# Kernel tuning notes

Measured on AMD Instinct MI355X. Metric: run time of the kernel, lower is better.

The kernel has to match this reference:

```python
import jax, jax.numpy as jnp
import numpy as np

EPS = 1e-5

def _rms(x, w):
    # RMSNorm over last dim (head_dim), affine weight w
    v = jnp.mean(jnp.square(x), axis=-1, keepdims=True)
    return x * jax.lax.rsqrt(v + EPS) * w

def _rope(x, cos, sin):
    # x: [B, N, H, D]; cos/sin: [N, D] (interleaved-pair convention)
    xr = x.reshape(*x.shape[:-1], -1, 2)
    rot = jnp.stack([-xr[..., 1], xr[..., 0]], axis=-1).reshape(x.shape)
    return x * cos[None, :, None, :] + rot * sin[None, :, None, :]

def _rope_tables(n, d):
    pos = np.arange(n, dtype=np.float32)
    freqs = 1.0 / (10000.0 ** (np.arange(0, d, 2, dtype=np.float32) / d))
    ang = pos[:, None] * freqs[None, :]          # [n, d/2]
    ang = np.repeat(ang, 2, axis=1)              # [n, d] interleaved pairs
    return jnp.asarray(np.cos(ang)), jnp.asarray(np.sin(ang))

def setup_inputs() -> dict:
    key = jax.random.key(0)
    ks = jax.random.split(key, 6)
    B, N1, N2, C, H, D = 2, 1536, 512, 1024, 16, 64
    cos1, sin1 = _rope_tables(N1, D)
    cos2, sin2 = _rope_tables(N2, D)
    s = 0.02
    return dict(
        seq_len=N1,
        x=jax.random.normal(ks[0], (B, N1, C), jnp.float32),
        y=jax.random.normal(ks[1], (B, N2, C), jnp.float32),
        cos1=cos1, sin1=sin1, cos2=cos2, sin2=sin2,
        W_qkv_xs=jax.random.normal(ks[2], (3 * C, C), jnp.float32) * s,
        W_qkv_au=jax.random.normal(ks[3], (3 * C, C), jnp.float32) * s,
        xs_q_w=jnp.ones((D,), jnp.float32), xs_k_w=jnp.ones((D,), jnp.float32),
        au_q_w=jnp.ones((D,), jnp.float32), au_k_w=jnp.ones((D,), jnp.float32),
        W_xs_proj=jax.random.normal(ks[4], (C, C), jnp.float32) * s,
        b_xs_proj=jnp.zeros((C,), jnp.float32),
        W_au_proj=jax.random.normal(ks[5], (C, C), jnp.float32) * s,
        b_au_proj=jnp.zeros((C,), jnp.float32),
    )

def reference(seq_len, x, y, cos1, sin1, cos2, sin2,
              W_qkv_xs, W_qkv_au, xs_q_w, xs_k_w, au_q_w, au_k_w,
              W_xs_proj, b_xs_proj, W_au_proj, b_au_proj):
    B, N1, C = x.shape
    N2 = y.shape[1]
    D = xs_q_w.shape[0]
    H = C // D
    scale = D ** -0.5

    # visual stream: QKV -> per-head RMSNorm -> RoPE
    xq, xk, xv = jnp.split(x @ W_qkv_xs.T, 3, axis=-1)          # each [B,N1,C]
    xq = _rms(xq.reshape(B, N1, H, D), xs_q_w)
    xk = _rms(xk.reshape(B, N1, H, D), xs_k_w)
    xv = xv.reshape(B, N1, H, D).transpose(0, 2, 1, 3)           # [B,H,N1,D]
    xq = _rope(xq, cos1, sin1).transpose(0, 2, 1, 3)             # [B,H,N1,D]
    xk = _rope(xk, cos1, sin1).transpose(0, 2, 1, 3)

    # audio stream: QKV -> per-head RMSNorm -> RoPE
    aq, ak, av = jnp.split(y @ W_qkv_au.T, 3, axis=-1)
    aq = _rms(aq.reshape(B, N2, H, D), au_q_w)
    ak = _rms(ak.reshape(B, N2, H, D), au_k_w)
    av = av.reshape(B, N2, H, D).transpose(0, 2, 1, 3)           # [B,H,N2,D]
    aq = _rope(aq, cos2, sin2).transpose(0, 2, 1, 3)             # [B,H,N2,D]
    ak = _rope(ak, cos2, sin2).transpose(0, 2, 1, 3)

    # joint attention over concatenated sequence
    q = jnp.concatenate([xq, aq], axis=2)                        # [B,H,N1+N2,D]
    k = jnp.concatenate([xk, ak], axis=2)
    v = jnp.concatenate([xv, av], axis=2)
    attn = jax.nn.softmax(jnp.einsum('bhqd,bhkd->bhqk', q * scale, k), axis=-1)
    o = jnp.einsum('bhqk,bhkd->bhqd', attn, v)
    o = o.transpose(0, 2, 1, 3).reshape(B, N1 + N2, C)

    xs = o[:, :N1] @ W_xs_proj.T + b_xs_proj
    au = o[:, N1:] @ W_au_proj.T + b_au_proj
    return xs, au
```

## Files before the change

kernel.cpp:

```cpp
#include <hip/hip_runtime.h>
#include <hip/hip_bf16.h>

typedef __bf16 bf16_t;
typedef bf16_t bf16x4_t __attribute__((ext_vector_type(4)));
typedef bf16_t bf16x8_t __attribute__((ext_vector_type(8)));
typedef float f32x4_t __attribute__((ext_vector_type(4)));
typedef float f32x16_t __attribute__((ext_vector_type(16)));

constexpr int kB = 2, kN1 = 1536, kN2 = 512, kN = 2048, kC = 1024, kH = 16, kD = 64;
constexpr int BK = 64, LDT = 72;

__device__ inline uint32_t pack2bf(float a, float b) {
  union { bf16_t h[2]; uint32_t u; } t;
  t.h[0] = (bf16_t)a; t.h[1] = (bf16_t)b;
  return t.u;
}
__device__ inline void pl32_swap(uint32_t& a, uint32_t& b) {
  asm volatile("v_permlane32_swap_b32 %0, %1" : "+v"(a), "+v"(b));
}
__device__ __forceinline__ void gl16(const bf16_t* g, bf16_t* l) {
  __builtin_amdgcn_global_load_lds(
      (const __attribute__((address_space(1))) unsigned int*)g,
      (__attribute__((address_space(3))) unsigned int*)l, 16, 0, 0);
}

__global__ __launch_bounds__(256)
void cvt_bf16(const float* __restrict__ x, const float* __restrict__ y,
              const float* __restrict__ wqx, const float* __restrict__ wqa,
              const float* __restrict__ wpx, const float* __restrict__ wpa,
              bf16_t* __restrict__ Xb, bf16_t* __restrict__ Wq, bf16_t* __restrict__ Wp)
{
  const int bid = blockIdx.x;
  const float* src; bf16_t* dst; size_t off;
  if (bid < 192)      { src = x;   dst = Xb;           off = (size_t)bid * 16384; }
  else if (bid < 256) { src = y;   dst = Xb + 3145728; off = (size_t)(bid - 192) * 16384; }
  else if (bid < 448) { src = wqx; dst = Wq;           off = (size_t)(bid - 256) * 16384; }
  else if (bid < 640) { src = wqa; dst = Wq + 3145728; off = (size_t)(bid - 448) * 16384; }
  else if (bid < 704) { src = wpx; dst = Wp;           off = (size_t)(bid - 640) * 16384; }
  else                { src = wpa; dst = Wp + 1048576; off = (size_t)(bid - 704) * 16384; }
  src += off; dst += off;
  const int t = threadIdx.x;
  #pragma unroll
  for (int i = 0; i < 16; ++i) {
    const int e = (t + i * 256) * 4;
    f32x4_t v = *(const f32x4_t*)(src + e);
    bf16x4_t o;
    #pragma unroll
    for (int j = 0; j < 4; ++j) o[j] = (bf16_t)v[j];
    *(bf16x4_t*)(dst + e) = o;
  }
}

__global__ __launch_bounds__(256, 2)
void qkv_gemm(const bf16_t* __restrict__ Xb, const bf16_t* __restrict__ Wq,
              const float* __restrict__ cos1, const float* __restrict__ sin1,
              const float* __restrict__ cos2, const float* __restrict__ sin2,
              const float* __restrict__ xs_qw, const float* __restrict__ xs_kw,
              const float* __restrict__ au_qw, const float* __restrict__ au_kw,
              bf16_t* __restrict__ Qb, bf16_t* __restrict__ Kb, bf16_t* __restrict__ Vt)
{
  __shared__ __align__(16) bf16_t smem[32768];
  const int tid = threadIdx.x, lane = tid & 63, w = tid >> 6;
  const int wr = w >> 1, wc = w & 1;
  const int bm = blockIdx.x, bn = blockIdx.y;
  const int l15 = lane & 15, l4 = (lane >> 4) & 3;
  const int K = kC;
  const bool is_xs = bm < 24;

  const bf16_t* Ag = Xb + (size_t)bm * 128 * K;
  const bf16_t* Bg = Wq + (is_xs ? (size_t)0 : (size_t)3072 * 1024) + (size_t)bn * 128 * K;

  const int srow_l = lane >> 3;
  const int scc = (((lane & 7) ^ ((lane >> 3) & 7)) << 3);

  auto stage = [&](int c, int kt) {
    const int k0 = kt * BK;
    bf16_t* Ab = smem + c * 8192;
    bf16_t* Bb = smem + 16384 + c * 8192;
    #pragma unroll
    for (int i = 0; i < 4; ++i) {
      const int row = w * 32 + i * 8 + srow_l;
      gl16(Ag + (size_t)row * K + k0 + scc, Ab + (w * 32 + i * 8) * 64);
      gl16(Bg + (size_t)row * K + k0 + scc, Bb + (w * 32 + i * 8) * 64);
    }
  };

  f32x4_t acc[4][4] = {};
  const int nk = K / BK;
  stage(0, 0);
  asm volatile("s_waitcnt vmcnt(0)" ::: "memory");
  __syncthreads();

  int cur = 0;
  for (int kt = 0; kt < nk; ++kt) {
    if (kt + 1 < nk) stage(cur ^ 1, kt + 1);
    const bf16_t* Ab = smem + cur * 8192;
    const bf16_t* Bb = smem + 16384 + cur * 8192;
    #pragma unroll
    for (int kk = 0; kk < 2; ++kk) {
      bf16x8_t a[4], b[4];
      #pragma unroll
      for (int m = 0; m < 4; ++m) {
        const int row = wr * 64 + m * 16 + l15;
        const int cc = (kk * 32 + l4 * 8) ^ ((row & 7) << 3);
        a[m] = *(const bf16x8_t*)&Ab[row * 64 + cc];
      }
      #pragma unroll
      for (int n = 0; n < 4; ++n) {
        const int row = wc * 64 + n * 16 + l15;
        const int cc = (kk * 32 + l4 * 8) ^ ((row & 7) << 3);
        b[n] = *(const bf16x8_t*)&Bb[row * 64 + cc];
      }
      #pragma unroll
      for (int m = 0; m < 4; ++m)
        #pragma unroll
        for (int n = 0; n < 4; ++n)
          acc[m][n] = __builtin_amdgcn_mfma_f32_16x16x32_bf16(a[m], b[n], acc[m][n], 0, 0, 0);
    }
    asm volatile("s_waitcnt vmcnt(0)" ::: "memory");
    __syncthreads();
    cur ^= 1;
  }

  const int sec = bn >> 3;
  const int grow0 = bm * 128;
  int b, n0, seq_off; const float* cT; const float* sT;
  if (is_xs) { b = grow0 / 1536; n0 = grow0 - b * 1536; seq_off = 0; cT = cos1; sT = sin1; }
  else { const int g2 = grow0 - 3072; b = g2 >> 9; n0 = g2 & 511; seq_off = 1536; cT = cos2; sT = sin2; }
  const int h = (bn & 7) * 2 + wc;

  if (sec < 2) {
    const float* wsel = is_xs ? (sec == 0 ? xs_qw : xs_kw) : (sec == 0 ? au_qw : au_kw);
    float wv[4];
    #pragma unroll
    for (int n = 0; n < 4; ++n) wv[n] = wsel[n * 16 + l15];
    bf16_t* Out = (sec == 0 ? Qb : Kb) + (((size_t)b * kH + h) * kN + seq_off + n0) * kD;
    const float qscale = (sec == 0) ? 0.125f * 1.44269504088896f : 1.0f;
    #pragma unroll
    for (int m = 0; m < 4; ++m)
      #pragma unroll
      for (int r = 0; r < 4; ++r) {
        const int rl = wr * 64 + m * 16 + l4 * 4 + r;
        float ss = 0.0f;
        #pragma unroll
        for (int n = 0; n < 4; ++n) ss += acc[m][n][r] * acc[m][n][r];
        ss += __shfl_xor(ss, 1); ss += __shfl_xor(ss, 2);
        ss += __shfl_xor(ss, 4); ss += __shfl_xor(ss, 8);
        const float rinv = rsqrtf(ss * (1.0f / 64.0f) + 1e-5f);
        const int nrow = n0 + rl;
        #pragma unroll
        for (int n = 0; n < 4; ++n) {
          const int dd = n * 16 + l15;
          const float xn = acc[m][n][r] * rinv * wv[n];
          const float partner = __shfl_xor(xn, 1);
          if (!(l15 & 1)) {
            const float c = cT[(size_t)nrow * 64 + dd];
            const float s = sT[(size_t)nrow * 64 + dd];
            const float ve = (xn * c - partner * s) * qscale;
            const float vo = (partner * c + xn * s) * qscale;
            *(uint32_t*)&Out[(size_t)rl * kD + dd] = pack2bf(ve, vo);
          }
        }
      }
  } else {
    bf16_t* Lt = smem;
    #pragma unroll
    for (int m = 0; m < 4; ++m)
      #pragma unroll
      for (int n = 0; n < 4; ++n) {
        const int col = wc * 64 + n * 16 + l15;
        #pragma unroll
        for (int j = 0; j < 2; ++j) {
          const int row = wr * 64 + m * 16 + l4 * 4 + j * 2;
          *(uint32_t*)&Lt[col * 136 + row] = pack2bf(acc[m][n][j * 2], acc[m][n][j * 2 + 1]);
        }
      }
    __syncthreads();
    const int seg = tid >> 1, half = tid & 1;
    const int hl = seg >> 6, dd = seg & 63;
    bf16_t* Vo = Vt + (((size_t)b * kH + (bn & 7) * 2 + hl) * kD + dd) * kN
                 + seq_off + n0 + half * 64;
    #pragma unroll
    for (int jj = 0; jj < 8; ++jj)
      *(bf16x8_t*)&Vo[jj * 8] = *(const bf16x8_t*)&Lt[seg * 136 + half * 64 + jj * 8];
  }
}

__global__ __launch_bounds__(256, 2)
void proj_gemm(const bf16_t* __restrict__ Ob, const bf16_t* __restrict__ Wp,
               const float* __restrict__ bxs, const float* __restrict__ bau,
               float* __restrict__ out)
{
  __shared__ __align__(16) bf16_t smem[32768];
  const int tid = threadIdx.x, lane = tid & 63, w = tid >> 6;
  const int wr = w >> 1, wc = w & 1;
  const int bm = blockIdx.x, bn = blockIdx.y;
  const int l15 = lane & 15, l4 = (lane >> 4) & 3;
  const int K = kC, N = kC;

  const int grow = bm * 128;
  const int b = grow >> 11, n0r = grow & 2047;
  const bf16_t* Bg; const float* bias; float* Cg;
  if (n0r < kN1) { Bg = Wp; bias = bxs; Cg = out + ((size_t)b * kN1 + n0r) * kC; }
  else { Bg = Wp + (size_t)1024 * 1024; bias = bau;
         Cg = out + (size_t)kB * kN1 * kC + ((size_t)b * kN2 + (n0r - kN1)) * kC; }
  Bg += (size_t)bn * 128 * K;
  const bf16_t* Ag = Ob + (size_t)grow * K;

  const int srow_l = lane >> 3;
  const int scc = (((lane & 7) ^ ((lane >> 3) & 7)) << 3);

  auto stage = [&](int c, int kt) {
    const int k0 = kt * BK;
    bf16_t* Ab = smem + c * 8192;
    bf16_t* Bb = smem + 16384 + c * 8192;
    #pragma unroll
    for (int i = 0; i < 4; ++i) {
      const int row = w * 32 + i * 8 + srow_l;
      gl16(Ag + (size_t)row * K + k0 + scc, Ab + (w * 32 + i * 8) * 64);
      gl16(Bg + (size_t)row * K + k0 + scc, Bb + (w * 32 + i * 8) * 64);
    }
  };

  f32x4_t acc[4][4] = {};
  const int nk = K / BK;
  stage(0, 0);
  asm volatile("s_waitcnt vmcnt(0)" ::: "memory");
  __syncthreads();

  int cur = 0;
  for (int kt = 0; kt < nk; ++kt) {
    if (kt + 1 < nk) stage(cur ^ 1, kt + 1);
    const bf16_t* Ab = smem + cur * 8192;
    const bf16_t* Bb = smem + 16384 + cur * 8192;
    #pragma unroll
    for (int kk = 0; kk < 2; ++kk) {
      bf16x8_t a[4], bfr[4];
      #pragma unroll
      for (int m = 0; m < 4; ++m) {
        const int row = wr * 64 + m * 16 + l15;
        const int cc = (kk * 32 + l4 * 8) ^ ((row & 7) << 3);
        a[m] = *(const bf16x8_t*)&Ab[row * 64 + cc];
      }
      #pragma unroll
      for (int n = 0; n < 4; ++n) {
        const int row = wc * 64 + n * 16 + l15;
        const int cc = (kk * 32 + l4 * 8) ^ ((row & 7) << 3);
        bfr[n] = *(const bf16x8_t*)&Bb[row * 64 + cc];
      }
      #pragma unroll
      for (int m = 0; m < 4; ++m)
        #pragma unroll
        for (int n = 0; n < 4; ++n)
          acc[m][n] = __builtin_amdgcn_mfma_f32_16x16x32_bf16(a[m], bfr[n], acc[m][n], 0, 0, 0);
    }
    asm volatile("s_waitcnt vmcnt(0)" ::: "memory");
    __syncthreads();
    cur ^= 1;
  }

  float bv[4];
  #pragma unroll
  for (int n = 0; n < 4; ++n) bv[n] = bias[bn * 128 + wc * 64 + n * 16 + l15];
  #pragma unroll
  for (int m = 0; m < 4; ++m)
    #pragma unroll
    for (int n = 0; n < 4; ++n) {
      const int col = bn * 128 + wc * 64 + n * 16 + l15;
      #pragma unroll
      for (int r = 0; r < 4; ++r) {
        const int row = wr * 64 + m * 16 + l4 * 4 + r;
        Cg[(size_t)row * N + col] = acc[m][n][r] + bv[n];
      }
    }
}

__global__ __launch_bounds__(512, 2)
void flash_attn(const bf16_t* __restrict__ Q, const bf16_t* __restrict__ K,
                const bf16_t* __restrict__ Vt, bf16_t* __restrict__ O)
{
  __shared__ __align__(16) bf16_t smem[18432];
  const int tid = threadIdx.x, lane = tid & 63, w = tid >> 6;
  const int l31 = lane & 31, hi8 = ((lane >> 5) << 3), hi4 = ((lane >> 5) << 2);
  const int lin = blockIdx.x;
  const int qt = lin >> 5, hid = lin & 31;
  const int h = hid & 15, b = hid >> 4;
  const size_t headoff = ((size_t)(b * kH + h)) * kN * kD;
  const bf16_t* Kg = K + headoff;
  const bf16_t* Vg = Vt + headoff;

  bf16x8_t qf[4];
  {
    const bf16_t* Qg = Q + headoff + (size_t)(qt * 256 + w * 32 + l31) * kD + hi8;
    #pragma unroll
    for (int ks = 0; ks < 4; ++ks) qf[ks] = *(const bf16x8_t*)(Qg + ks * 16);
  }
  bf16x8_t onesv;
  #pragma unroll
  for (int j = 0; j < 8; ++j) onesv[j] = (bf16_t)1.0f;

  const int srow = tid >> 3, sc = (tid & 7) * 8;
  bf16x8_t kreg = *(const bf16x8_t*)(Kg + srow * kD + sc);
  bf16x8_t vreg = *(const bf16x8_t*)(Vg + (size_t)srow * kN + sc);

  f32x16_t oA0 = {}, oA1 = {}, accl = {};

  for (int kt = 0; kt < kN / 64; ++kt) {
    const int cur = kt & 1;
    bf16_t* Kc = smem + cur * 4608;
    bf16_t* Vc = smem + 9216 + cur * 4608;
    *(bf16x8_t*)&Kc[srow * LDT + sc] = kreg;
    *(bf16x8_t*)&Vc[srow * LDT + sc] = vreg;
    if (kt + 1 < kN / 64) {
      kreg = *(const bf16x8_t*)(Kg + (size_t)(kt + 1) * 64 * kD + srow * kD + sc);
      vreg = *(const bf16x8_t*)(Vg + (size_t)srow * kN + (kt + 1) * 64 + sc);
    }
    __syncthreads();

    f32x16_t s0 = {}, s1 = {};
    #pragma unroll
    for (int ks = 0; ks < 4; ++ks) {
      bf16x8_t k0 = *(const bf16x8_t*)&Kc[l31 * LDT + ks * 16 + hi8];
      bf16x8_t k1 = *(const bf16x8_t*)&Kc[(32 + l31) * LDT + ks * 16 + hi8];
      s0 = __builtin_amdgcn_mfma_f32_32x32x16_bf16(k0, qf[ks], s0, 0, 0, 0);
      s1 = __builtin_amdgcn_mfma_f32_32x32x16_bf16(k1, qf[ks], s1, 0, 0, 0);
    }

    #pragma unroll
    for (int i = 0; i < 16; ++i) {
      s0[i] = __builtin_amdgcn_exp2f(s0[i]);
      s1[i] = __builtin_amdgcn_exp2f(s1[i]);
    }

    union PW { uint32_t wd[4]; bf16x8_t v; } pf[4];
    #pragma unroll
    for (int o = 0; o < 2; ++o) {
      #pragma unroll
      for (int hh = 0; hh < 2; ++hh) {
        const int h8 = hh * 8, ks = o * 2 + hh;
        float p0, p1, p2, p3, p4, p5, p6, p7;
        if (o == 0) {
          p0 = s0[h8+0]; p1 = s0[h8+1]; p2 = s0[h8+2]; p3 = s0[h8+3];
          p4 = s0[h8+4]; p5 = s0[h8+5]; p6 = s0[h8+6]; p7 = s0[h8+7];
        } else {
          p0 = s1[h8+0]; p1 = s1[h8+1]; p2 = s1[h8+2]; p3 = s1[h8+3];
          p4 = s1[h8+4]; p5 = s1[h8+5]; p6 = s1[h8+6]; p7 = s1[h8+7];
        }
        uint32_t xw  = pack2bf(p0, p1), x2 = pack2bf(p2, p3);
        uint32_t yw  = pack2bf(p4, p5), y2 = pack2bf(p6, p7);
        pl32_swap(xw, yw);
        pl32_swap(x2, y2);
        pf[ks].wd[0] = xw; pf[ks].wd[1] = x2; pf[ks].wd[2] = yw; pf[ks].wd[3] = y2;
      }
    }

    #pragma unroll
    for (int ks = 0; ks < 4; ++ks) {
      bf16x8_t v0 = *(const bf16x8_t*)&Vc[l31 * LDT + ks * 16 + hi8];
      bf16x8_t v1 = *(const bf16x8_t*)&Vc[(32 + l31) * LDT + ks * 16 + hi8];
      oA0 = __builtin_amdgcn_mfma_f32_32x32x16_bf16(v0, pf[ks].v, oA0, 0, 0, 0);
      oA1 = __builtin_amdgcn_mfma_f32_32x32x16_bf16(v1, pf[ks].v, oA1, 0, 0, 0);
      accl = __builtin_amdgcn_mfma_f32_32x32x16_bf16(onesv, pf[ks].v, accl, 0, 0, 0);
    }
  }

  __syncthreads();
  bf16_t* Ow = smem + w * 2304;
  const float inv = 1.0f / accl[0];
  #pragma unroll
  for (int db = 0; db < 2; ++db) {
    f32x16_t o = db ? oA1 : oA0;
    #pragma unroll
    for (int rp = 0; rp < 8; ++rp) {
      const int d = db * 32 + ((rp & 1) << 1) + ((rp >> 1) << 3) + hi4;
      *(uint32_t*)&Ow[l31 * LDT + d] = pack2bf(o[2 * rp] * inv, o[2 * rp + 1] * inv);
    }
  }
  const int rq = lane >> 1, half = lane & 1;
  bf16x8_t r0 = *(const bf16x8_t*)&Ow[rq * LDT + half * 32];
  bf16x8_t r1 = *(const bf16x8_t*)&Ow[rq * LDT + half * 32 + 8];
  bf16x8_t r2 = *(const bf16x8_t*)&Ow[rq * LDT + half * 32 + 16];
  bf16x8_t r3 = *(const bf16x8_t*)&Ow[rq * LDT + half * 32 + 24];
  bf16_t* Og = O + ((size_t)b * kN + qt * 256 + w * 32 + rq) * kC + h * kD + half * 32;
  *(bf16x8_t*)&Og[0]  = r0;
  *(bf16x8_t*)&Og[8]  = r1;
  *(bf16x8_t*)&Og[16] = r2;
  *(bf16x8_t*)&Og[24] = r3;
}

extern "C" void kernel_launch(void* const* d_in, const int* in_sizes, int n_in,
                              void* d_out, int out_size, void* d_ws, size_t ws_size,
                              hipStream_t stream) {
  const float* x    = (const float*)d_in[1];
  const float* y    = (const float*)d_in[2];
  const float* cos1 = (const float*)d_in[3];
  const float* sin1 = (const float*)d_in[4];
  const float* cos2 = (const float*)d_in[5];
  const float* sin2 = (const float*)d_in[6];
  const float* Wqkv_xs = (const float*)d_in[7];
  const float* Wqkv_au = (const float*)d_in[8];
  const float* xs_q_w  = (const float*)d_in[9];
  const float* xs_k_w  = (const float*)d_in[10];
  const float* au_q_w  = (const float*)d_in[11];
  const float* au_k_w  = (const float*)d_in[12];
  const float* Wxs = (const float*)d_in[13];
  const float* bxs = (const float*)d_in[14];
  const float* Wau = (const float*)d_in[15];
  const float* bau = (const float*)d_in[16];
  float* out = (float*)d_out;

  char* ws = (char*)d_ws;
  bf16_t* Xb = (bf16_t*)(ws);
  bf16_t* Wq = (bf16_t*)(ws + 8388608);
  bf16_t* Wp = (bf16_t*)(ws + 20971520);
  bf16_t* Qb = (bf16_t*)(ws + 25165824);
  bf16_t* Kb = (bf16_t*)(ws + 33554432);
  bf16_t* Vt = (bf16_t*)(ws + 41943040);
  bf16_t* Ob = (bf16_t*)(ws + 50331648);

  cvt_bf16<<<dim3(768), dim3(256), 0, stream>>>(x, y, Wqkv_xs, Wqkv_au, Wxs, Wau, Xb, Wq, Wp);
  qkv_gemm<<<dim3(32, 24), dim3(256), 0, stream>>>(Xb, Wq, cos1, sin1, cos2, sin2,
      xs_q_w, xs_k_w, au_q_w, au_k_w, Qb, Kb, Vt);
  flash_attn<<<dim3(256), dim3(512), 0, stream>>>(Qb, Kb, Vt, Ob);
  proj_gemm<<<dim3(32, 8), dim3(256), 0, stream>>>(Ob, Wp, bxs, bau, out);
}
```

Before: 128.2 us.

## Triple-buffer GEMM LDS staging with partial vmcnt waits and single barrier

Both QKV and projection GEMMs move from double to triple buffering in LDS, prefetching two K-tiles ahead and waiting only until the oldest tile's loads complete (vmcnt(8)) before a single barrier per iteration. This is meant to hide global-load latency and remove the full drain plus second barrier each iteration. LDS use grows from 64KB to 96KB per block, which may limit the two-blocks-per-CU occupancy. The attention kernel swaps __syncthreads for an explicit lgkmcnt wait, raw s_barrier and a sched_barrier.

```diff
diff --git a/kernel.cpp b/kernel.cpp
--- a/kernel.cpp
+++ b/kernel.cpp
@@ -59,7 +59,7 @@
               const float* __restrict__ au_qw, const float* __restrict__ au_kw,
               bf16_t* __restrict__ Qb, bf16_t* __restrict__ Kb, bf16_t* __restrict__ Vt)
 {
-  __shared__ __align__(16) bf16_t smem[32768];
+  __shared__ __align__(16) bf16_t smem[49152];
   const int tid = threadIdx.x, lane = tid & 63, w = tid >> 6;
   const int wr = w >> 1, wc = w & 1;
   const int bm = blockIdx.x, bn = blockIdx.y;
@@ -76,7 +76,7 @@
   auto stage = [&](int c, int kt) {
     const int k0 = kt * BK;
     bf16_t* Ab = smem + c * 8192;
-    bf16_t* Bb = smem + 16384 + c * 8192;
+    bf16_t* Bb = smem + 24576 + c * 8192;
     #pragma unroll
     for (int i = 0; i < 4; ++i) {
       const int row = w * 32 + i * 8 + srow_l;
@@ -88,14 +88,18 @@
   f32x4_t acc[4][4] = {};
   const int nk = K / BK;
   stage(0, 0);
-  asm volatile("s_waitcnt vmcnt(0)" ::: "memory");
-  __syncthreads();
-
-  int cur = 0;
+  stage(1, 1);
+
   for (int kt = 0; kt < nk; ++kt) {
-    if (kt + 1 < nk) stage(cur ^ 1, kt + 1);
+    if (kt == nk - 1) asm volatile("s_waitcnt vmcnt(0)" ::: "memory");
+    else              asm volatile("s_waitcnt vmcnt(8)" ::: "memory");
+    __builtin_amdgcn_s_barrier();
+    __builtin_amdgcn_sched_barrier(0);
+    if (kt + 2 < nk) stage((kt + 2) % 3, kt + 2);
+
+    const int cur = kt % 3;
     const bf16_t* Ab = smem + cur * 8192;
-    const bf16_t* Bb = smem + 16384 + cur * 8192;
+    const bf16_t* Bb = smem + 24576 + cur * 8192;
     #pragma unroll
     for (int kk = 0; kk < 2; ++kk) {
       bf16x8_t a[4], b[4];
@@ -117,10 +121,8 @@
         for (int n = 0; n < 4; ++n)
           acc[m][n] = __builtin_amdgcn_mfma_f32_16x16x32_bf16(a[m], b[n], acc[m][n], 0, 0, 0);
     }
-    asm volatile("s_waitcnt vmcnt(0)" ::: "memory");
-    __syncthreads();
-    cur ^= 1;
-  }
+  }
+  __builtin_amdgcn_s_barrier();
 
   const int sec = bn >> 3;
   const int grow0 = bm * 128;
@@ -191,7 +193,7 @@
                const float* __restrict__ bxs, const float* __restrict__ bau,
                float* __restrict__ out)
 {
-  __shared__ __align__(16) bf16_t smem[32768];
+  __shared__ __align__(16) bf16_t smem[49152];
   const int tid = threadIdx.x, lane = tid & 63, w = tid >> 6;
   const int wr = w >> 1, wc = w & 1;
   const int bm = blockIdx.x, bn = blockIdx.y;
@@ -213,7 +215,7 @@
   auto stage = [&](int c, int kt) {
     const int k0 = kt * BK;
     bf16_t* Ab = smem + c * 8192;
-    bf16_t* Bb = smem + 16384 + c * 8192;
+    bf16_t* Bb = smem + 24576 + c * 8192;
     #pragma unroll
     for (int i = 0; i < 4; ++i) {
       const int row = w * 32 + i * 8 + srow_l;
@@ -225,14 +227,18 @@
   f32x4_t acc[4][4] = {};
   const int nk = K / BK;
   stage(0, 0);
-  asm volatile("s_waitcnt vmcnt(0)" ::: "memory");
-  __syncthreads();
-
-  int cur = 0;
+  stage(1, 1);
+
   for (int kt = 0; kt < nk; ++kt) {
-    if (kt + 1 < nk) stage(cur ^ 1, kt + 1);
+    if (kt == nk - 1) asm volatile("s_waitcnt vmcnt(0)" ::: "memory");
+    else              asm volatile("s_waitcnt vmcnt(8)" ::: "memory");
+    __builtin_amdgcn_s_barrier();
+    __builtin_amdgcn_sched_barrier(0);
+    if (kt + 2 < nk) stage((kt + 2) % 3, kt + 2);
+
+    const int cur = kt % 3;
     const bf16_t* Ab = smem + cur * 8192;
-    const bf16_t* Bb = smem + 16384 + cur * 8192;
+    const bf16_t* Bb = smem + 24576 + cur * 8192;
     #pragma unroll
     for (int kk = 0; kk < 2; ++kk) {
       bf16x8_t a[4], bfr[4];
@@ -254,9 +260,6 @@
         for (int n = 0; n < 4; ++n)
           acc[m][n] = __builtin_amdgcn_mfma_f32_16x16x32_bf16(a[m], bfr[n], acc[m][n], 0, 0, 0);
     }
-    asm volatile("s_waitcnt vmcnt(0)" ::: "memory");
-    __syncthreads();
-    cur ^= 1;
   }
 
   float bv[4];
@@ -315,7 +318,9 @@
       kreg = *(const bf16x8_t*)(Kg + (size_t)(kt + 1) * 64 * kD + srow * kD + sc);
       vreg = *(const bf16x8_t*)(Vg + (size_t)srow * kN + (kt + 1) * 64 + sc);
     }
-    __syncthreads();
+    asm volatile("s_waitcnt lgkmcnt(0)" ::: "memory");
+    __builtin_amdgcn_s_barrier();
+    __builtin_amdgcn_sched_barrier(0);
 
     f32x16_t s0 = {}, s1 = {};
     #pragma unroll
```

After: 155.6 us. 1.21x slower.

## Triple-buffer QKV GEMM with BK=32 and partial vmcnt waits

Applied to the files above, without the earlier changes.

Restructures the QKV GEMM main loop from double-buffered BK=64 stages to a three-stage ring of BK=32 tiles. Loads run two stages ahead, and each iteration waits only on the older loads (vmcnt(4)) before the barrier, so global loads overlap MFMA work more deeply. The smaller LDS footprint allows 3 blocks per CU through launch bounds. In exchange there are twice as many barriers per K step, less MFMA work between syncs, and possible register pressure from the higher occupancy target.

```diff
diff --git a/kernel.cpp b/kernel.cpp
--- a/kernel.cpp
+++ b/kernel.cpp
@@ -51,7 +51,7 @@
   }
 }
 
-__global__ __launch_bounds__(256, 2)
+__global__ __launch_bounds__(256, 3)
 void qkv_gemm(const bf16_t* __restrict__ Xb, const bf16_t* __restrict__ Wq,
               const float* __restrict__ cos1, const float* __restrict__ sin1,
               const float* __restrict__ cos2, const float* __restrict__ sin2,
@@ -59,7 +59,7 @@
               const float* __restrict__ au_qw, const float* __restrict__ au_kw,
               bf16_t* __restrict__ Qb, bf16_t* __restrict__ Kb, bf16_t* __restrict__ Vt)
 {
-  __shared__ __align__(16) bf16_t smem[32768];
+  __shared__ __align__(16) bf16_t smem[24576];
   const int tid = threadIdx.x, lane = tid & 63, w = tid >> 6;
   const int wr = w >> 1, wc = w & 1;
   const int bm = blockIdx.x, bn = blockIdx.y;
@@ -70,57 +70,56 @@
   const bf16_t* Ag = Xb + (size_t)bm * 128 * K;
   const bf16_t* Bg = Wq + (is_xs ? (size_t)0 : (size_t)3072 * 1024) + (size_t)bn * 128 * K;
 
-  const int srow_l = lane >> 3;
-  const int scc = (((lane & 7) ^ ((lane >> 3) & 7)) << 3);
+  const int srow32 = lane >> 2;
+  const int scc32 = (((lane & 3) ^ ((lane >> 2) & 3)) << 3);
 
   auto stage = [&](int c, int kt) {
-    const int k0 = kt * BK;
-    bf16_t* Ab = smem + c * 8192;
-    bf16_t* Bb = smem + 16384 + c * 8192;
-    #pragma unroll
-    for (int i = 0; i < 4; ++i) {
-      const int row = w * 32 + i * 8 + srow_l;
-      gl16(Ag + (size_t)row * K + k0 + scc, Ab + (w * 32 + i * 8) * 64);
-      gl16(Bg + (size_t)row * K + k0 + scc, Bb + (w * 32 + i * 8) * 64);
+    const int k0 = kt * 32;
+    bf16_t* Ab = smem + c * 4096;
+    bf16_t* Bb = smem + 12288 + c * 4096;
+    #pragma unroll
+    for (int i = 0; i < 2; ++i) {
+      const int row = w * 32 + i * 16 + srow32;
+      gl16(Ag + (size_t)row * K + k0 + scc32, Ab + (w * 32 + i * 16) * 32);
+      gl16(Bg + (size_t)row * K + k0 + scc32, Bb + (w * 32 + i * 16) * 32);
     }
   };
 
   f32x4_t acc[4][4] = {};
-  const int nk = K / BK;
+  const int nk = K / 32;
   stage(0, 0);
-  asm volatile("s_waitcnt vmcnt(0)" ::: "memory");
-  __syncthreads();
-
-  int cur = 0;
+  stage(1, 1);
+
   for (int kt = 0; kt < nk; ++kt) {
-    if (kt + 1 < nk) stage(cur ^ 1, kt + 1);
-    const bf16_t* Ab = smem + cur * 8192;
-    const bf16_t* Bb = smem + 16384 + cur * 8192;
-    #pragma unroll
-    for (int kk = 0; kk < 2; ++kk) {
-      bf16x8_t a[4], b[4];
-      #pragma unroll
-      for (int m = 0; m < 4; ++m) {
-        const int row = wr * 64 + m * 16 + l15;
-        const int cc = (kk * 32 + l4 * 8) ^ ((row & 7) << 3);
-        a[m] = *(const bf16x8_t*)&Ab[row * 64 + cc];
-      }
-      #pragma unroll
-      for (int n = 0; n < 4; ++n) {
-        const int row = wc * 64 + n * 16 + l15;
-        const int cc = (kk * 32 + l4 * 8) ^ ((row & 7) << 3);
-        b[n] = *(const bf16x8_t*)&Bb[row * 64 + cc];
-      }
-      #pragma unroll
-      for (int m = 0; m < 4; ++m)
-        #pragma unroll
-        for (int n = 0; n < 4; ++n)
-          acc[m][n] = __builtin_amdgcn_mfma_f32_16x16x32_bf16(a[m], b[n], acc[m][n], 0, 0, 0);
-    }
-    asm volatile("s_waitcnt vmcnt(0)" ::: "memory");
-    __syncthreads();
-    cur ^= 1;
-  }
+    if (kt >= nk - 2) asm volatile("s_waitcnt vmcnt(0)" ::: "memory");
+    else              asm volatile("s_waitcnt vmcnt(4)" ::: "memory");
+    __builtin_amdgcn_s_barrier();
+    __builtin_amdgcn_sched_barrier(0);
+    if (kt + 2 < nk) stage((kt + 2) % 3, kt + 2);
+
+    const int cur = kt % 3;
+    const bf16_t* Ab = smem + cur * 4096;
+    const bf16_t* Bb = smem + 12288 + cur * 4096;
+    bf16x8_t a[4], b[4];
+    #pragma unroll
+    for (int m = 0; m < 4; ++m) {
+      const int row = wr * 64 + m * 16 + l15;
+      const int cc = (l4 * 8) ^ ((row & 3) << 3);
+      a[m] = *(const bf16x8_t*)&Ab[row * 32 + cc];
+    }
+    #pragma unroll
+    for (int n = 0; n < 4; ++n) {
+      const int row = wc * 64 + n * 16 + l15;
+      const int cc = (l4 * 8) ^ ((row & 3) << 3);
+      b[n] = *(const bf16x8_t*)&Bb[row * 32 + cc];
+    }
+    #pragma unroll
+    for (int m = 0; m < 4; ++m)
+      #pragma unroll
+      for (int n = 0; n < 4; ++n)
+        acc[m][n] = __builtin_amdgcn_mfma_f32_16x16x32_bf16(a[m], b[n], acc[m][n], 0, 0, 0);
+  }
+  __builtin_amdgcn_s_barrier();
 
   const int sec = bn >> 3;
   const int grow0 = bm * 128;
```

After: 125.3 us. 1.02x faster.
